# Optimization experiments

Measured on AMD Instinct MI355X. Metric: run time of the kernel, lower is better.

## Reference

```python
import jax, jax.numpy as jnp
import numpy as np

B, T, IN, HID, G = 64, 500, 1024, 1024, 8
IG = IN // G   # per-group input size = 128
HG = HID // G  # per-group hidden size = 128


def setup_inputs() -> dict:
    key = jax.random.key(0)
    k0, k1, k2, k3, k4 = jax.random.split(key, 5)
    s = 1.0 / np.sqrt(HG)  # torch GRU init: U(-1/sqrt(hidden), 1/sqrt(hidden))
    x = jax.random.normal(k0, (B, T, IN), dtype=jnp.float32)
    W_ih = jax.random.uniform(k1, (G, 3 * HG, IG), jnp.float32, -s, s)  # gate order r,z,n
    W_hh = jax.random.uniform(k2, (G, 3 * HG, HG), jnp.float32, -s, s)
    b_ih = jax.random.uniform(k3, (G, 3 * HG), jnp.float32, -s, s)
    b_hh = jax.random.uniform(k4, (G, 3 * HG), jnp.float32, -s, s)
    return {"x": x, "W_ih": W_ih, "W_hh": W_hh, "b_ih": b_ih, "b_hh": b_hh}


def reference(x, W_ih, W_hh, b_ih, b_hh):
    b, t, _ = x.shape
    g, h3, ig = W_ih.shape
    hg = h3 // 3
    xg = x.reshape(b, t, g, ig)  # split channels into groups
    # precompute input projections for all timesteps/groups: [B,T,G,3*HG]
    xp = jnp.einsum('btgi,gji->btgj', xg, W_ih) + b_ih
    h0 = jnp.zeros((b, g, hg), x.dtype)

    def step(h, xt):
        # h: [B,G,HG], xt: [B,G,3*HG]
        hp = jnp.einsum('bgh,gjh->bgj', h, W_hh) + b_hh
        xr, xz, xn = jnp.split(xt, 3, axis=-1)
        hr, hz, hn = jnp.split(hp, 3, axis=-1)
        r = jax.nn.sigmoid(xr + hr)
        z = jax.nn.sigmoid(xz + hz)
        n = jnp.tanh(xn + r * hn)
        h_new = (1.0 - z) * n + z * h
        return h_new, h_new

    _, hs = jax.lax.scan(step, h0, jnp.moveaxis(xp, 1, 0))  # hs: [T,B,G,HG]
    out = jnp.moveaxis(hs, 0, 1).reshape(b, t, g * hg)  # concat groups on last dim
    return out
```

## Files before the change

### kernel.cpp

```cpp
#include <hip/hip_runtime.h>
#include <math.h>

#define B_   64
#define T_   500
#define IN_  1024
#define G_   8
#define HG_  128
#define J3_  384

typedef _Float16 half8 __attribute__((ext_vector_type(8)));
typedef _Float16 half4 __attribute__((ext_vector_type(4)));
typedef float    f32x4 __attribute__((ext_vector_type(4)));

#define S_RZ (-1.44269504f)
#define S_N  (-2.88539008f)

static __device__ __forceinline__ half8 cvt_half8_s(const float* p, float s) {
    const float4 a = *(const float4*)p;
    const float4 b = *(const float4*)(p + 4);
    half8 h;
    h[0]=(_Float16)(a.x*s); h[1]=(_Float16)(a.y*s); h[2]=(_Float16)(a.z*s); h[3]=(_Float16)(a.w*s);
    h[4]=(_Float16)(b.x*s); h[5]=(_Float16)(b.y*s); h[6]=(_Float16)(b.z*s); h[7]=(_Float16)(b.w*s);
    return h;
}

static __device__ __forceinline__ void pin_frag(half8& h) {
    f32x4 t = __builtin_bit_cast(f32x4, h);
    float a = t[0], b = t[1], c = t[2], d = t[3];
    asm volatile("" : "+v"(a), "+v"(b), "+v"(c), "+v"(d));
    t[0] = a; t[1] = b; t[2] = c; t[3] = d;
    h = __builtin_bit_cast(half8, t);
}
static __device__ __forceinline__ void pin_f32x4(f32x4& v) {
    float a = v[0], b = v[1], c = v[2], d = v[3];
    asm volatile("" : "+v"(a), "+v"(b), "+v"(c), "+v"(d));
    v[0] = a; v[1] = b; v[2] = c; v[3] = d;
}

static __device__ __forceinline__ void barrier_lds_only() {
    asm volatile("s_waitcnt lgkmcnt(0)\n\ts_barrier" ::: "memory");
}

static __device__ __forceinline__ float sel4(f32x4 v, int rsel) {
    const float t0 = (rsel & 1) ? v[1] : v[0];
    const float t1 = (rsel & 1) ? v[3] : v[2];
    return (rsel & 2) ? t1 : t0;
}

#define MFMA16(A,Bv,C) __builtin_amdgcn_mfma_f32_16x16x32_f16((A),(Bv),(C),0,0,0)

__global__ __launch_bounds__(256)
void cvt_x(const float* __restrict__ x, _Float16* __restrict__ x16)
{
    const size_t n4 = (size_t)B_ * T_ * IN_ / 4;
    const size_t stride = (size_t)gridDim.x * 256;
    for (size_t i = (size_t)blockIdx.x * 256 + threadIdx.x; i < n4; i += stride) {
        const float4 v = ((const float4*)x)[i];
        half4 h;
        h[0] = (_Float16)v.x; h[1] = (_Float16)v.y;
        h[2] = (_Float16)v.z; h[3] = (_Float16)v.w;
        ((half4*)x16)[i] = h;
    }
}

__global__ __launch_bounds__(512, 1)
void gru_fused(const float* __restrict__ Wih, const float* __restrict__ Whh,
               const float* __restrict__ bih, const float* __restrict__ bhh,
               const _Float16* __restrict__ x16, float* __restrict__ out)
{
    const int tid  = threadIdx.x;
    const int lane = tid & 63;
    const int w    = tid >> 6;
    const int lr   = lane & 15;
    const int hi   = lane >> 4;
    const int blk  = blockIdx.x;
    const int g    = blk & 7;
    const int bp   = blk >> 3;
    const int sq   = lr & 1;
    const int rsel = (lr >> 1) & 3;
    const int jl   = w * 16 + hi * 4;
    const int jown = jl + rsel;
    const int bown = bp * 2 + sq;

    __shared__ _Float16 h16[2][2][HG_];
    __shared__ float    xmem[16][392];

    half8 aI[3][4], aH[3][4];
#pragma unroll
    for (int p = 0; p < 3; ++p)
#pragma unroll
        for (int kt = 0; kt < 4; ++kt) {
            const size_t roff = (size_t)(g * J3_ + p * 128 + w * 16 + lr) * HG_
                              + kt * 32 + hi * 8;
            const float s = (p == 2) ? S_N : S_RZ;
            aI[p][kt] = cvt_half8_s(Wih + roff, s);  pin_frag(aI[p][kt]);
            aH[p][kt] = cvt_half8_s(Whh + roff, s);  pin_frag(aH[p][kt]);
        }

    const float* bi = bih + g * J3_;
    const float* bh = bhh + g * J3_;
    f32x4 s0 = (*(const f32x4*)(bi + jl)       + *(const f32x4*)(bh + jl))       * S_RZ;
    f32x4 s1 = (*(const f32x4*)(bi + 128 + jl) + *(const f32x4*)(bh + 128 + jl)) * S_RZ;
    f32x4 s2 = (*(const f32x4*)(bi + 256 + jl)) * S_N;
    f32x4 bhn_s = (*(const f32x4*)(bh + 256 + jl)) * S_N;
    pin_f32x4(s0); pin_f32x4(s1); pin_f32x4(s2); pin_f32x4(bhn_s);

    float hreg = 0.f;
    if (tid < 256) h16[0][tid >> 7][tid & 127] = (_Float16)0.f;

    const _Float16* xcol = x16 + (size_t)(bp * 2 + (lr & 1)) * T_ * IN_ + g * HG_;
    float*          oown = out + (size_t)bown * T_ * IN_ + g * HG_ + jown;

    half8 bx[4];
    {
        const _Float16* px = xcol + (size_t)(lr >> 1) * IN_;
#pragma unroll
        for (int kt = 0; kt < 4; ++kt) bx[kt] = *(const half8*)(px + kt * 32 + hi * 8);
    }

    __syncthreads();

#define REC_STEP(S)                                                                \
    do {                                                                           \
        const int pb = (S) & 1;                                                    \
                \
        const _Float16* hsrc = &h16[pb][sq][0];                                    \
        const half8 bf0 = *(const half8*)(hsrc +  0 + hi * 8);                     \
        const half8 bf1 = *(const half8*)(hsrc + 32 + hi * 8);                     \
        const half8 bf2 = *(const half8*)(hsrc + 64 + hi * 8);                     \
        const half8 bf3 = *(const half8*)(hsrc + 96 + hi * 8);                     \
                    \
        const int xc = (S) * 2 + sq;                                               \
        const f32x4 xa0 = *(const f32x4*)&xmem[xc][      jl];                      \
        const f32x4 xa1 = *(const f32x4*)&xmem[xc][128 + jl];                      \
        const f32x4 xa2 = *(const f32x4*)&xmem[xc][256 + jl];                      \
                   \
        f32x4 h0 = xa0, h1 = xa1, h2 = bhn_s;                                      \
        h0 = MFMA16(aH[0][0], bf0, h0);                                            \
        h1 = MFMA16(aH[1][0], bf0, h1);                                            \
        h2 = MFMA16(aH[2][0], bf0, h2);                                            \
        h0 = MFMA16(aH[0][1], bf1, h0);                                            \
        h1 = MFMA16(aH[1][1], bf1, h1);                                            \
        h2 = MFMA16(aH[2][1], bf1, h2);                                            \
        h0 = MFMA16(aH[0][2], bf2, h0);                                            \
        h1 = MFMA16(aH[1][2], bf2, h1);                                            \
        h2 = MFMA16(aH[2][2], bf2, h2);                                            \
        h0 = MFMA16(aH[0][3], bf3, h0);                                            \
        h1 = MFMA16(aH[1][3], bf3, h1);                                            \
        h2 = MFMA16(aH[2][3], bf3, h2);                                            \
                        \
        const float ar = sel4(h0, rsel);                       \
        const float az = sel4(h1, rsel);                       \
        const float an = sel4(h2, rsel);                        \
        const float xn = sel4(xa2, rsel);                       \
        const float rg = __builtin_amdgcn_rcpf(1.f + __builtin_amdgcn_exp2f(ar));  \
        const float zg = __builtin_amdgcn_rcpf(1.f + __builtin_amdgcn_exp2f(az));  \
        const float pre = xn + rg * an;                                            \
        const float th  = __builtin_fmaf(2.f,                                      \
            __builtin_amdgcn_rcpf(1.f + __builtin_amdgcn_exp2f(pre)), -1.f);       \
        const float hnew = __builtin_fmaf(zg, hreg - th, th);                      \
        hreg = hnew;                                                               \
                                \
        if (lr < 8) {                                                              \
            h16[pb ^ 1][sq][jown] = (_Float16)hnew;                                \
            oown[(size_t)(t0 + (S)) * IN_] = hnew;                                 \
        }                                                                          \
        barrier_lds_only();                                                        \
    } while (0)

    for (int t0 = 0; t0 < T_; t0 += 8) {
        {
            f32x4 d0 = s0, d1 = s1, d2 = s2;
#pragma unroll
            for (int kt = 0; kt < 4; ++kt) {
                d0 = MFMA16(aI[0][kt], bx[kt], d0);
                d1 = MFMA16(aI[1][kt], bx[kt], d1);
                d2 = MFMA16(aI[2][kt], bx[kt], d2);
            }
            *(f32x4*)&xmem[lr][      w * 16 + hi * 4] = d0;
            *(f32x4*)&xmem[lr][128 + w * 16 + hi * 4] = d1;
            *(f32x4*)&xmem[lr][256 + w * 16 + hi * 4] = d2;
            int tn = t0 + 8 + (lr >> 1); if (tn > T_ - 1) tn = T_ - 1;
            const _Float16* px = xcol + (size_t)tn * IN_;
#pragma unroll
            for (int kt = 0; kt < 4; ++kt) bx[kt] = *(const half8*)(px + kt * 32 + hi * 8);
        }
        REC_STEP(0); REC_STEP(1); REC_STEP(2); REC_STEP(3);
        if (t0 + 4 < T_) {
            REC_STEP(4); REC_STEP(5); REC_STEP(6); REC_STEP(7);
        }
    }
#undef REC_STEP
}

extern "C" void kernel_launch(void* const* d_in, const int* in_sizes, int n_in,
                              void* d_out, int out_size, void* d_ws, size_t ws_size,
                              hipStream_t stream) {
    (void)in_sizes; (void)n_in; (void)out_size; (void)ws_size;
    const float* x   = (const float*)d_in[0];
    const float* Wih = (const float*)d_in[1];
    const float* Whh = (const float*)d_in[2];
    const float* bih = (const float*)d_in[3];
    const float* bhh = (const float*)d_in[4];
    float* out = (float*)d_out;

    _Float16* x16 = (_Float16*)d_ws;

    cvt_x<<<4096, 256, 0, stream>>>(x, x16);
    gru_fused<<<256, 512, 0, stream>>>(Wih, Whh, bih, bhh, x16, out);
}
```

Baseline: 267.9 us.

## Interleave input-projection MFMAs into recurrent steps and prefetch next-step xmem reads

The input projection for the next 8-step chunk no longer runs as a separate block before each chunk. Its 12 MFMAs are spread across steps 0-3 of the recurrence and written into a double-buffered xmem, so they can fill gaps in the serial recurrent chain. Each step also loads the next step's xmem slice into registers early, taking LDS latency off the critical path. The cost is more registers and added control logic, and correctness now depends on the double-buffer index and the barrier ordering.

Measured after the change: 260.1 us. -2.9%, faster.

```diff
diff --git a/kernel.cpp b/kernel.cpp
--- a/kernel.cpp
+++ b/kernel.cpp
@@ -83,7 +83,7 @@
     const int bown = bp * 2 + sq;
 
     __shared__ _Float16 h16[2][2][HG_];
-    __shared__ float    xmem[16][392];
+    __shared__ float    xmem[2][16][392];
 
     half8 aI[3][4], aH[3][4];
 #pragma unroll
@@ -117,25 +117,54 @@
 #pragma unroll
         for (int kt = 0; kt < 4; ++kt) bx[kt] = *(const half8*)(px + kt * 32 + hi * 8);
     }
+    {
+        f32x4 d0 = s0, d1 = s1, d2 = s2;
+#pragma unroll
+        for (int kt = 0; kt < 4; ++kt) {
+            d0 = MFMA16(aI[0][kt], bx[kt], d0);
+            d1 = MFMA16(aI[1][kt], bx[kt], d1);
+            d2 = MFMA16(aI[2][kt], bx[kt], d2);
+        }
+        *(f32x4*)&xmem[0][lr][      w * 16 + hi * 4] = d0;
+        *(f32x4*)&xmem[0][lr][128 + w * 16 + hi * 4] = d1;
+        *(f32x4*)&xmem[0][lr][256 + w * 16 + hi * 4] = d2;
+    }
+    {
+        int tn = 8 + (lr >> 1); if (tn > T_ - 1) tn = T_ - 1;
+        const _Float16* px = xcol + (size_t)tn * IN_;
+#pragma unroll
+        for (int kt = 0; kt < 4; ++kt) bx[kt] = *(const half8*)(px + kt * 32 + hi * 8);
+    }
+    f32x4 pxa0, pxa1, pxa2;
+    {
+        const int xc = sq;
+        pxa0 = *(const f32x4*)&xmem[0][xc][      jl];
+        pxa1 = *(const f32x4*)&xmem[0][xc][128 + jl];
+        pxa2 = *(const f32x4*)&xmem[0][xc][256 + jl];
+    }
+    f32x4 d0, d1, d2;
 
     __syncthreads();
 
 #define REC_STEP(S)                                                                \
     do {                                                                           \
         const int pb = (S) & 1;                                                    \
-                \
+                                                \
         const _Float16* hsrc = &h16[pb][sq][0];                                    \
         const half8 bf0 = *(const half8*)(hsrc +  0 + hi * 8);                     \
         const half8 bf1 = *(const half8*)(hsrc + 32 + hi * 8);                     \
         const half8 bf2 = *(const half8*)(hsrc + 64 + hi * 8);                     \
         const half8 bf3 = *(const half8*)(hsrc + 96 + hi * 8);                     \
-                    \
-        const int xc = (S) * 2 + sq;                                               \
-        const f32x4 xa0 = *(const f32x4*)&xmem[xc][      jl];                      \
-        const f32x4 xa1 = *(const f32x4*)&xmem[xc][128 + jl];                      \
-        const f32x4 xa2 = *(const f32x4*)&xmem[xc][256 + jl];                      \
-                   \
-        f32x4 h0 = xa0, h1 = xa1, h2 = bhn_s;                                      \
+               \
+                  \
+        if ((S) == 0) { d0 = s0; d1 = s1; d2 = s2; }                               \
+        if ((S) < 4) {                                                             \
+            d0 = MFMA16(aI[0][(S) & 3], bx[(S) & 3], d0);                          \
+            d1 = MFMA16(aI[1][(S) & 3], bx[(S) & 3], d1);                          \
+            d2 = MFMA16(aI[2][(S) & 3], bx[(S) & 3], d2);                          \
+        }                                                                          \
+                      \
+        f32x4 h0 = pxa0, h1 = pxa1, h2 = bhn_s;                                    \
         h0 = MFMA16(aH[0][0], bf0, h0);                                            \
         h1 = MFMA16(aH[1][0], bf0, h1);                                            \
         h2 = MFMA16(aH[2][0], bf0, h2);                                            \
@@ -148,11 +177,31 @@
         h0 = MFMA16(aH[0][3], bf3, h0);                                            \
         h1 = MFMA16(aH[1][3], bf3, h1);                                            \
         h2 = MFMA16(aH[2][3], bf3, h2);                                            \
+                    \
+        if ((S) == 3) {                                                            \
+            *(f32x4*)&xmem[xb ^ 1][lr][      w * 16 + hi * 4] = d0;                \
+            *(f32x4*)&xmem[xb ^ 1][lr][128 + w * 16 + hi * 4] = d1;                \
+            *(f32x4*)&xmem[xb ^ 1][lr][256 + w * 16 + hi * 4] = d2;                \
+            int tn = t0 + 16 + (lr >> 1); if (tn > T_ - 1) tn = T_ - 1;            \
+            const _Float16* px = xcol + (size_t)tn * IN_;                          \
+            bx[0] = *(const half8*)(px +  0 + hi * 8);                             \
+            bx[1] = *(const half8*)(px + 32 + hi * 8);                             \
+            bx[2] = *(const half8*)(px + 64 + hi * 8);                             \
+            bx[3] = *(const half8*)(px + 96 + hi * 8);                             \
+        }                                                                          \
+                            \
+        {                                                                          \
+            const int nxb = ((S) == 7) ? (xb ^ 1) : xb;                            \
+            const int nxc = (((S) + 1) & 7) * 2 + sq;                              \
+            pxa0 = *(const f32x4*)&xmem[nxb][nxc][      jl];                       \
+            pxa1 = *(const f32x4*)&xmem[nxb][nxc][128 + jl];                       \
+            pxa2 = *(const f32x4*)&xmem[nxb][nxc][256 + jl];                       \
+        }                                                                          \
                         \
-        const float ar = sel4(h0, rsel);                       \
-        const float az = sel4(h1, rsel);                       \
-        const float an = sel4(h2, rsel);                        \
-        const float xn = sel4(xa2, rsel);                       \
+        const float ar = sel4(h0, rsel);                                           \
+        const float az = sel4(h1, rsel);                                           \
+        const float an = sel4(h2, rsel);                                           \
+        const float xn = xn_cur;                                                   \
         const float rg = __builtin_amdgcn_rcpf(1.f + __builtin_amdgcn_exp2f(ar));  \
         const float zg = __builtin_amdgcn_rcpf(1.f + __builtin_amdgcn_exp2f(az));  \
         const float pre = xn + rg * an;                                            \
@@ -169,25 +218,19 @@
     } while (0)
 
     for (int t0 = 0; t0 < T_; t0 += 8) {
+        const int xb = (t0 >> 3) & 1;
         {
-            f32x4 d0 = s0, d1 = s1, d2 = s2;
-#pragma unroll
-            for (int kt = 0; kt < 4; ++kt) {
-                d0 = MFMA16(aI[0][kt], bx[kt], d0);
-                d1 = MFMA16(aI[1][kt], bx[kt], d1);
-                d2 = MFMA16(aI[2][kt], bx[kt], d2);
-            }
-            *(f32x4*)&xmem[lr][      w * 16 + hi * 4] = d0;
-            *(f32x4*)&xmem[lr][128 + w * 16 + hi * 4] = d1;
-            *(f32x4*)&xmem[lr][256 + w * 16 + hi * 4] = d2;
-            int tn = t0 + 8 + (lr >> 1); if (tn > T_ - 1) tn = T_ - 1;
-            const _Float16* px = xcol + (size_t)tn * IN_;
-#pragma unroll
-            for (int kt = 0; kt < 4; ++kt) bx[kt] = *(const half8*)(px + kt * 32 + hi * 8);
-        }
-        REC_STEP(0); REC_STEP(1); REC_STEP(2); REC_STEP(3);
+            float xn_cur = sel4(pxa2, rsel);
+            REC_STEP(0);
+        }
+        { float xn_cur = sel4(pxa2, rsel); REC_STEP(1); }
+        { float xn_cur = sel4(pxa2, rsel); REC_STEP(2); }
+        { float xn_cur = sel4(pxa2, rsel); REC_STEP(3); }
         if (t0 + 4 < T_) {
-            REC_STEP(4); REC_STEP(5); REC_STEP(6); REC_STEP(7);
+            { float xn_cur = sel4(pxa2, rsel); REC_STEP(4); }
+            { float xn_cur = sel4(pxa2, rsel); REC_STEP(5); }
+            { float xn_cur = sel4(pxa2, rsel); REC_STEP(6); }
+            { float xn_cur = sel4(pxa2, rsel); REC_STEP(7); }
         }
     }
 #undef REC_STEP
```
